# Kernel optimization log

Measured on AMD Instinct MI355X. Metric: run time of the kernel, lower is better.

The kernel has to match this reference:

```python
import jax, jax.numpy as jnp
import numpy as np

B, H, S, D = 2, 16, 2048, 64


def setup_inputs() -> dict:
    key = jax.random.key(0)
    kq, kk, kv = jax.random.split(key, 3)
    q = jax.random.normal(kq, (B, H, S, D), dtype=jnp.float32)
    k = jax.random.normal(kk, (B, H, S, D), dtype=jnp.float32)
    v = jax.random.normal(kv, (B, H, S, D), dtype=jnp.float32)
    # look-ahead (causal) mask: 1 where attention is NOT allowed (future positions)
    mask = 1.0 - jnp.tril(jnp.ones((S, S), dtype=jnp.float32))
    mask = mask[None, None, :, :]  # broadcastable to (B, H, S, S)
    return {"q": q, "k": k, "v": v, "mask": mask}


def reference(q, k, v, mask):
    # scores: (B, H, Sq, Sk)
    dk = jnp.asarray(q.shape[-1], dtype=q.dtype)
    logits = jnp.einsum("bhqd,bhkd->bhqk", q, k) / jnp.sqrt(dk)
    logits = logits + mask * (-1e9)
    attn = jax.nn.softmax(logits, axis=-1)
    # dropout rate 0.0 / inference mode -> identity
    out = jnp.einsum("bhqk,bhkd->bhqd", attn, v)
    return out, attn
```

## Files before the change

### kernel.cpp

```cpp
#include <hip/hip_runtime.h>


typedef __attribute__((ext_vector_type(4))) float f32x4;
typedef __attribute__((ext_vector_type(8))) short bf16x8;

#define S_LEN 2048
#define D_DIM 64
#define LDK   72
#define SCALE2 0.18033688f

__device__ __forceinline__ unsigned int f2bf1(float f) {
  unsigned int u = __float_as_uint(f);
  return (u + 0x7FFFu + ((u >> 16) & 1u)) >> 16;
}
__device__ __forceinline__ unsigned long long pack4bf(float a, float b, float c, float d) {
  unsigned int lo = f2bf1(a) | (f2bf1(b) << 16);
  unsigned int hi = f2bf1(c) | (f2bf1(d) << 16);
  return (unsigned long long)lo | ((unsigned long long)hi << 32);
}

__global__ __launch_bounds__(256, 2)
void attn_fused(const float* __restrict__ Qg, const float* __restrict__ Kg,
                const float* __restrict__ Vg, float* __restrict__ Og,
                float* __restrict__ Ag)
{
  __shared__ __attribute__((aligned(16))) unsigned short qs[64 * LDK];
  __shared__ __attribute__((aligned(16))) unsigned short ks[2][64 * LDK];
  __shared__ __attribute__((aligned(16))) unsigned short vs[2][64 * LDK];

  const int tid  = threadIdx.x;
  const int w    = tid >> 6;
  const int l15  = tid & 15;
  const int lg   = (tid >> 4) & 3;
  const int bh   = blockIdx.x & 31;
  const int pj   = blockIdx.x >> 5;

  const float* qb = Qg + (size_t)bh * S_LEN * D_DIM;
  const float* kb = Kg + (size_t)bh * S_LEN * D_DIM;
  const float* vb = Vg + (size_t)bh * S_LEN * D_DIM;
  float* ob = Og + (size_t)bh * S_LEN * D_DIM;
  float* ab = Ag + (size_t)bh * S_LEN * S_LEN;

  unsigned short* pw = qs + w * 16 * LDK;

  for (int sel = 0; sel < 2; ++sel) {
    const int jq   = sel ? (31 - pj) : pj;
    const int q0   = jq << 6;
    const int T    = jq + 1;
    const int qrow = q0 + w * 16 + l15;
    const int qr0  = q0 + w * 16 + lg * 4;

    __syncthreads();
#pragma unroll
    for (int jj = 0; jj < 4; ++jj) {
      int f = tid + jj * 256;
      int row = f >> 4, dg = f & 15;
      float4 v = *(const float4*)(qb + (q0 + row) * D_DIM + dg * 4);
      *(unsigned long long*)(qs + row * LDK + dg * 4) = pack4bf(v.x, v.y, v.z, v.w);
    }
#pragma unroll
    for (int jj = 0; jj < 4; ++jj) {
      int f = tid + jj * 256;
      int row = f >> 4, dg = f & 15;
      float4 v = *(const float4*)(kb + row * D_DIM + dg * 4);
      *(unsigned long long*)(ks[0] + row * LDK + dg * 4) = pack4bf(v.x, v.y, v.z, v.w);
    }
    __syncthreads();
    const bf16x8 qf0 = *(const bf16x8*)(qs + (w * 16 + l15) * LDK + lg * 8);
    const bf16x8 qf1 = *(const bf16x8*)(qs + (w * 16 + l15) * LDK + 32 + lg * 8);

    float lsum = 0.f;
    int cur = 0;

#define P1_KBK(MASKED)                                                                  \
    _Pragma("unroll")                                                                   \
    for (int kbk = 0; kbk < 4; ++kbk) {                                                 \
      const bf16x8 kf0 = *(const bf16x8*)(kcur + (kbk * 16 + l15) * LDK + lg * 8);      \
      const bf16x8 kf1 = *(const bf16x8*)(kcur + (kbk * 16 + l15) * LDK + 32 + lg * 8); \
      f32x4 s = {0.f, 0.f, 0.f, 0.f};                                                   \
      s = __builtin_amdgcn_mfma_f32_16x16x32_bf16(kf0, qf0, s, 0, 0, 0);                \
      s = __builtin_amdgcn_mfma_f32_16x16x32_bf16(kf1, qf1, s, 0, 0, 0);                \
      _Pragma("unroll")                                                                 \
      for (int r = 0; r < 4; ++r) {                                                     \
        float e = exp2f(s[r] * SCALE2);                                                 \
        if (MASKED) lsum += (kt + kbk * 16 + lg * 4 + r <= qrow) ? e : 0.f;             \
        else        lsum += e;                                                          \
      }                                                                                 \
    }

    for (int t = 0; t < T; ++t) {
      const int kt = t << 6;
      const bool pf = (t + 1 < T);
      float4 kl[4];
      if (pf) {
#pragma unroll
        for (int jj = 0; jj < 4; ++jj) {
          int f = tid + jj * 256;
          int row = f >> 4, dg = f & 15;
          kl[jj] = *(const float4*)(kb + (kt + 64 + row) * D_DIM + dg * 4);
        }
      }
      const unsigned short* kcur = ks[cur];
      if (t == T - 1) { P1_KBK(1) } else { P1_KBK(0) }
      if (pf) {
#pragma unroll
        for (int jj = 0; jj < 4; ++jj) {
          int f = tid + jj * 256;
          int row = f >> 4, dg = f & 15;
          *(unsigned long long*)(ks[cur ^ 1] + row * LDK + dg * 4) =
              pack4bf(kl[jj].x, kl[jj].y, kl[jj].z, kl[jj].w);
        }
      }
      __syncthreads();
      cur ^= 1;
    }
    lsum += __shfl_xor(lsum, 16, 64);
    lsum += __shfl_xor(lsum, 32, 64);
    const float ri = 1.f / lsum;

    f32x4 o[4];
#pragma unroll
    for (int d = 0; d < 4; ++d) o[d] = (f32x4){0.f, 0.f, 0.f, 0.f};

#pragma unroll
    for (int jj = 0; jj < 4; ++jj) {
      int f = tid + jj * 256;
      int row = f >> 4, dg = f & 15;
      float4 v = *(const float4*)(kb + row * D_DIM + dg * 4);
      *(unsigned long long*)(ks[0] + row * LDK + dg * 4) = pack4bf(v.x, v.y, v.z, v.w);
    }
    {
      const int kb4 = tid >> 4, db4 = tid & 15;
      const float* vsrc = vb + (kb4 * 4) * D_DIM + db4 * 4;
      float4 r0 = *(const float4*)(vsrc);
      float4 r1 = *(const float4*)(vsrc + D_DIM);
      float4 r2 = *(const float4*)(vsrc + 2 * D_DIM);
      float4 r3 = *(const float4*)(vsrc + 3 * D_DIM);
      *(unsigned long long*)(vs[0] + (db4 * 4 + 0) * LDK + kb4 * 4) = pack4bf(r0.x, r1.x, r2.x, r3.x);
      *(unsigned long long*)(vs[0] + (db4 * 4 + 1) * LDK + kb4 * 4) = pack4bf(r0.y, r1.y, r2.y, r3.y);
      *(unsigned long long*)(vs[0] + (db4 * 4 + 2) * LDK + kb4 * 4) = pack4bf(r0.z, r1.z, r2.z, r3.z);
      *(unsigned long long*)(vs[0] + (db4 * 4 + 3) * LDK + kb4 * 4) = pack4bf(r0.w, r1.w, r2.w, r3.w);
    }
    __syncthreads();

#define P2_KBK(MASKED)                                                                  \
    _Pragma("unroll")                                                                   \
    for (int kbk = 0; kbk < 4; ++kbk) {                                                 \
      const bf16x8 kf0 = *(const bf16x8*)(kcur + (kbk * 16 + l15) * LDK + lg * 8);      \
      const bf16x8 kf1 = *(const bf16x8*)(kcur + (kbk * 16 + l15) * LDK + 32 + lg * 8); \
      f32x4 s = {0.f, 0.f, 0.f, 0.f};                                                   \
      s = __builtin_amdgcn_mfma_f32_16x16x32_bf16(kf0, qf0, s, 0, 0, 0);                \
      s = __builtin_amdgcn_mfma_f32_16x16x32_bf16(kf1, qf1, s, 0, 0, 0);                \
      f32x4 pv;                                                                         \
      _Pragma("unroll")                                                                 \
      for (int r = 0; r < 4; ++r) {                                                     \
        float p = exp2f(s[r] * SCALE2) * ri;                                            \
        if (MASKED) p = (kt + kbk * 16 + lg * 4 + r <= qrow) ? p : 0.f;                 \
        pv[r] = p;                                                                      \
      }                                                                                 \
      __builtin_nontemporal_store(pv,                                                   \
        (f32x4*)(ab + (size_t)qrow * S_LEN + kt + kbk * 16 + lg * 4));                  \
      *(unsigned long long*)(pw + l15 * LDK + kbk * 16 + lg * 4) =                      \
          pack4bf(pv[0], pv[1], pv[2], pv[3]);                                          \
    }

    cur = 0;
    for (int t = 0; t < T; ++t) {
      const int kt = t << 6;
      const bool pf = (t + 1 < T);
      float4 kl[4], v0, v1, v2, v3;
      if (pf) {
#pragma unroll
        for (int jj = 0; jj < 4; ++jj) {
          int f = tid + jj * 256;
          int row = f >> 4, dg = f & 15;
          kl[jj] = *(const float4*)(kb + (kt + 64 + row) * D_DIM + dg * 4);
        }
        const int kb4 = tid >> 4, db4 = tid & 15;
        const float* vsrc = vb + (kt + 64 + kb4 * 4) * D_DIM + db4 * 4;
        v0 = *(const float4*)(vsrc);
        v1 = *(const float4*)(vsrc + D_DIM);
        v2 = *(const float4*)(vsrc + 2 * D_DIM);
        v3 = *(const float4*)(vsrc + 3 * D_DIM);
      }
      const unsigned short* kcur = ks[cur];
      if (t == T - 1) { P2_KBK(1) } else { P2_KBK(0) }
      asm volatile("s_waitcnt lgkmcnt(0)" ::: "memory");

      const bf16x8 pa0 = *(const bf16x8*)(pw + l15 * LDK + lg * 8);
      const bf16x8 pa1 = *(const bf16x8*)(pw + l15 * LDK + 32 + lg * 8);
      const unsigned short* vcur = vs[cur];
#pragma unroll
      for (int d = 0; d < 4; ++d) {
        const bf16x8 vf0 = *(const bf16x8*)(vcur + (d * 16 + l15) * LDK + lg * 8);
        const bf16x8 vf1 = *(const bf16x8*)(vcur + (d * 16 + l15) * LDK + 32 + lg * 8);
        o[d] = __builtin_amdgcn_mfma_f32_16x16x32_bf16(pa0, vf0, o[d], 0, 0, 0);
        o[d] = __builtin_amdgcn_mfma_f32_16x16x32_bf16(pa1, vf1, o[d], 0, 0, 0);
      }
      if (pf) {
#pragma unroll
        for (int jj = 0; jj < 4; ++jj) {
          int f = tid + jj * 256;
          int row = f >> 4, dg = f & 15;
          *(unsigned long long*)(ks[cur ^ 1] + row * LDK + dg * 4) =
              pack4bf(kl[jj].x, kl[jj].y, kl[jj].z, kl[jj].w);
        }
        const int kb4 = tid >> 4, db4 = tid & 15;
        *(unsigned long long*)(vs[cur ^ 1] + (db4 * 4 + 0) * LDK + kb4 * 4) = pack4bf(v0.x, v1.x, v2.x, v3.x);
        *(unsigned long long*)(vs[cur ^ 1] + (db4 * 4 + 1) * LDK + kb4 * 4) = pack4bf(v0.y, v1.y, v2.y, v3.y);
        *(unsigned long long*)(vs[cur ^ 1] + (db4 * 4 + 2) * LDK + kb4 * 4) = pack4bf(v0.z, v1.z, v2.z, v3.z);
        *(unsigned long long*)(vs[cur ^ 1] + (db4 * 4 + 3) * LDK + kb4 * 4) = pack4bf(v0.w, v1.w, v2.w, v3.w);
      }
      __syncthreads();
      cur ^= 1;
    }

    {
      const f32x4 z = (f32x4){0.f, 0.f, 0.f, 0.f};
#pragma unroll
      for (int jj = 0; jj < 4; ++jj) {
        const int zrow = q0 + w * 16 + jj * 4 + lg;
        float* rp = ab + (size_t)zrow * S_LEN;
        for (int c = q0 + 64 + l15 * 4; c < S_LEN; c += 64)
          __builtin_nontemporal_store(z, (f32x4*)(rp + c));
      }
    }

#pragma unroll
    for (int r = 0; r < 4; ++r) {
      float* rp = ob + (size_t)(qr0 + r) * D_DIM + l15;
      __builtin_nontemporal_store(o[0][r], rp);
      __builtin_nontemporal_store(o[1][r], rp + 16);
      __builtin_nontemporal_store(o[2][r], rp + 32);
      __builtin_nontemporal_store(o[3][r], rp + 48);
    }
  }
}

extern "C" void kernel_launch(void* const* d_in, const int* in_sizes, int n_in,
                              void* d_out, int out_size, void* d_ws, size_t ws_size,
                              hipStream_t stream) {
  (void)in_sizes; (void)n_in; (void)d_ws; (void)ws_size; (void)out_size;
  const float* q = (const float*)d_in[0];
  const float* k = (const float*)d_in[1];
  const float* v = (const float*)d_in[2];
  float* out  = (float*)d_out;
  float* attn = out + (size_t)2 * 16 * 2048 * 64;
  attn_fused<<<dim3(512), dim3(256), 0, stream>>>(q, k, v, out, attn);
}
```

Measured before the change: 170.3 us.

## Process both paired query tiles in one K/V sweep to share staged tiles

Each block now processes its two paired query tiles (pj and 31-pj) together in a single pass over the K and V tiles, instead of running the whole two-pass pipeline twice. Staged K/V tiles are loaded and converted once and serve both query tiles, which cuts global loads, bf16 conversions and barriers. The QK MFMA operand order is swapped so each lane's scores run along key columns, and the attention matrix is written as row-coalesced 16-byte stores read back from the bf16 P buffer in shared memory. It also remaps blockIdx to the pair index so heavy and light blocks interleave. The costs are roughly doubled register pressure (two accumulator sets and row sums) under launch bounds of 2 blocks per CU, and attention values are now stored rounded to bf16 rather than in fp32.

```diff
diff --git a/kernel.cpp b/kernel.cpp
--- a/kernel.cpp
+++ b/kernel.cpp
@@ -33,7 +33,17 @@
   const int l15  = tid & 15;
   const int lg   = (tid >> 4) & 3;
   const int bh   = blockIdx.x & 31;
-  const int pj   = blockIdx.x >> 5;
+  const int m    = blockIdx.x >> 5;
+  const int pj   = (m < 8) ? m : (23 - m);
+
+  const int jqA  = pj;
+  const int jqB  = 31 - pj;
+  const int q0A  = jqA << 6;
+  const int q0B  = jqB << 6;
+  const int TA   = jqA + 1;
+  const int TB   = jqB + 1;
+  const int qr0A = q0A + w * 16 + lg * 4;
+  const int qr0B = q0B + w * 16 + lg * 4;
 
   const float* qb = Qg + (size_t)bh * S_LEN * D_DIM;
   const float* kb = Kg + (size_t)bh * S_LEN * D_DIM;
@@ -43,197 +53,239 @@
 
   unsigned short* pw = qs + w * 16 * LDK;
 
-  for (int sel = 0; sel < 2; ++sel) {
-    const int jq   = sel ? (31 - pj) : pj;
-    const int q0   = jq << 6;
-    const int T    = jq + 1;
-    const int qrow = q0 + w * 16 + l15;
-    const int qr0  = q0 + w * 16 + lg * 4;
-
-    __syncthreads();
-#pragma unroll
-    for (int jj = 0; jj < 4; ++jj) {
-      int f = tid + jj * 256;
-      int row = f >> 4, dg = f & 15;
-      float4 v = *(const float4*)(qb + (q0 + row) * D_DIM + dg * 4);
-      *(unsigned long long*)(qs + row * LDK + dg * 4) = pack4bf(v.x, v.y, v.z, v.w);
-    }
-#pragma unroll
-    for (int jj = 0; jj < 4; ++jj) {
-      int f = tid + jj * 256;
-      int row = f >> 4, dg = f & 15;
-      float4 v = *(const float4*)(kb + row * D_DIM + dg * 4);
-      *(unsigned long long*)(ks[0] + row * LDK + dg * 4) = pack4bf(v.x, v.y, v.z, v.w);
-    }
-    __syncthreads();
-    const bf16x8 qf0 = *(const bf16x8*)(qs + (w * 16 + l15) * LDK + lg * 8);
-    const bf16x8 qf1 = *(const bf16x8*)(qs + (w * 16 + l15) * LDK + 32 + lg * 8);
-
-    float lsum = 0.f;
-    int cur = 0;
-
-#define P1_KBK(MASKED)                                                                  \
+#pragma unroll
+  for (int jj = 0; jj < 4; ++jj) {
+    int f = tid + jj * 256;
+    int row = f >> 4, dg = f & 15;
+    float4 v = *(const float4*)(qb + (q0A + row) * D_DIM + dg * 4);
+    *(unsigned long long*)(qs + row * LDK + dg * 4) = pack4bf(v.x, v.y, v.z, v.w);
+  }
+#pragma unroll
+  for (int jj = 0; jj < 4; ++jj) {
+    int f = tid + jj * 256;
+    int row = f >> 4, dg = f & 15;
+    float4 v = *(const float4*)(kb + row * D_DIM + dg * 4);
+    *(unsigned long long*)(ks[0] + row * LDK + dg * 4) = pack4bf(v.x, v.y, v.z, v.w);
+  }
+  __syncthreads();
+  const bf16x8 qfA0 = *(const bf16x8*)(qs + (w * 16 + l15) * LDK + lg * 8);
+  const bf16x8 qfA1 = *(const bf16x8*)(qs + (w * 16 + l15) * LDK + 32 + lg * 8);
+  __syncthreads();
+#pragma unroll
+  for (int jj = 0; jj < 4; ++jj) {
+    int f = tid + jj * 256;
+    int row = f >> 4, dg = f & 15;
+    float4 v = *(const float4*)(qb + (q0B + row) * D_DIM + dg * 4);
+    *(unsigned long long*)(qs + row * LDK + dg * 4) = pack4bf(v.x, v.y, v.z, v.w);
+  }
+  __syncthreads();
+  const bf16x8 qfB0 = *(const bf16x8*)(qs + (w * 16 + l15) * LDK + lg * 8);
+  const bf16x8 qfB1 = *(const bf16x8*)(qs + (w * 16 + l15) * LDK + 32 + lg * 8);
+
+#define P1_STEP(QF0, QF1, LSUM, QR0, MASKED)                                            \
+  {                                                                                     \
     _Pragma("unroll")                                                                   \
     for (int kbk = 0; kbk < 4; ++kbk) {                                                 \
       const bf16x8 kf0 = *(const bf16x8*)(kcur + (kbk * 16 + l15) * LDK + lg * 8);      \
       const bf16x8 kf1 = *(const bf16x8*)(kcur + (kbk * 16 + l15) * LDK + 32 + lg * 8); \
       f32x4 s = {0.f, 0.f, 0.f, 0.f};                                                   \
-      s = __builtin_amdgcn_mfma_f32_16x16x32_bf16(kf0, qf0, s, 0, 0, 0);                \
-      s = __builtin_amdgcn_mfma_f32_16x16x32_bf16(kf1, qf1, s, 0, 0, 0);                \
+      s = __builtin_amdgcn_mfma_f32_16x16x32_bf16(QF0, kf0, s, 0, 0, 0);                \
+      s = __builtin_amdgcn_mfma_f32_16x16x32_bf16(QF1, kf1, s, 0, 0, 0);                \
+      const int kc = kt + kbk * 16 + l15;                                               \
       _Pragma("unroll")                                                                 \
       for (int r = 0; r < 4; ++r) {                                                     \
         float e = exp2f(s[r] * SCALE2);                                                 \
-        if (MASKED) lsum += (kt + kbk * 16 + lg * 4 + r <= qrow) ? e : 0.f;             \
-        else        lsum += e;                                                          \
+        if (MASKED) LSUM[r] += (kc <= (QR0) + r) ? e : 0.f;                             \
+        else        LSUM[r] += e;                                                       \
       }                                                                                 \
-    }
-
-    for (int t = 0; t < T; ++t) {
-      const int kt = t << 6;
-      const bool pf = (t + 1 < T);
-      float4 kl[4];
-      if (pf) {
-#pragma unroll
-        for (int jj = 0; jj < 4; ++jj) {
-          int f = tid + jj * 256;
-          int row = f >> 4, dg = f & 15;
-          kl[jj] = *(const float4*)(kb + (kt + 64 + row) * D_DIM + dg * 4);
-        }
+    }                                                                                   \
+  }
+
+  float lsumA[4] = {0.f, 0.f, 0.f, 0.f};
+  float lsumB[4] = {0.f, 0.f, 0.f, 0.f};
+  int cur = 0;
+  for (int t = 0; t < TB; ++t) {
+    const int kt = t << 6;
+    const bool pf = (t + 1 < TB);
+    float4 kl[4];
+    if (pf) {
+#pragma unroll
+      for (int jj = 0; jj < 4; ++jj) {
+        int f = tid + jj * 256;
+        int row = f >> 4, dg = f & 15;
+        kl[jj] = *(const float4*)(kb + (kt + 64 + row) * D_DIM + dg * 4);
       }
-      const unsigned short* kcur = ks[cur];
-      if (t == T - 1) { P1_KBK(1) } else { P1_KBK(0) }
-      if (pf) {
-#pragma unroll
-        for (int jj = 0; jj < 4; ++jj) {
-          int f = tid + jj * 256;
-          int row = f >> 4, dg = f & 15;
-          *(unsigned long long*)(ks[cur ^ 1] + row * LDK + dg * 4) =
-              pack4bf(kl[jj].x, kl[jj].y, kl[jj].z, kl[jj].w);
-        }
+    }
+    const unsigned short* kcur = ks[cur];
+    if (t < TA) {
+      if (t == TA - 1) P1_STEP(qfA0, qfA1, lsumA, qr0A, 1)
+      else             P1_STEP(qfA0, qfA1, lsumA, qr0A, 0)
+    }
+    if (t == TB - 1) P1_STEP(qfB0, qfB1, lsumB, qr0B, 1)
+    else             P1_STEP(qfB0, qfB1, lsumB, qr0B, 0)
+    if (pf) {
+#pragma unroll
+      for (int jj = 0; jj < 4; ++jj) {
+        int f = tid + jj * 256;
+        int row = f >> 4, dg = f & 15;
+        *(unsigned long long*)(ks[cur ^ 1] + row * LDK + dg * 4) =
+            pack4bf(kl[jj].x, kl[jj].y, kl[jj].z, kl[jj].w);
       }
-      __syncthreads();
-      cur ^= 1;
-    }
-    lsum += __shfl_xor(lsum, 16, 64);
-    lsum += __shfl_xor(lsum, 32, 64);
-    const float ri = 1.f / lsum;
-
-    f32x4 o[4];
-#pragma unroll
-    for (int d = 0; d < 4; ++d) o[d] = (f32x4){0.f, 0.f, 0.f, 0.f};
-
-#pragma unroll
-    for (int jj = 0; jj < 4; ++jj) {
-      int f = tid + jj * 256;
-      int row = f >> 4, dg = f & 15;
-      float4 v = *(const float4*)(kb + row * D_DIM + dg * 4);
-      *(unsigned long long*)(ks[0] + row * LDK + dg * 4) = pack4bf(v.x, v.y, v.z, v.w);
-    }
-    {
-      const int kb4 = tid >> 4, db4 = tid & 15;
-      const float* vsrc = vb + (kb4 * 4) * D_DIM + db4 * 4;
-      float4 r0 = *(const float4*)(vsrc);
-      float4 r1 = *(const float4*)(vsrc + D_DIM);
-      float4 r2 = *(const float4*)(vsrc + 2 * D_DIM);
-      float4 r3 = *(const float4*)(vsrc + 3 * D_DIM);
-      *(unsigned long long*)(vs[0] + (db4 * 4 + 0) * LDK + kb4 * 4) = pack4bf(r0.x, r1.x, r2.x, r3.x);
-      *(unsigned long long*)(vs[0] + (db4 * 4 + 1) * LDK + kb4 * 4) = pack4bf(r0.y, r1.y, r2.y, r3.y);
-      *(unsigned long long*)(vs[0] + (db4 * 4 + 2) * LDK + kb4 * 4) = pack4bf(r0.z, r1.z, r2.z, r3.z);
-      *(unsigned long long*)(vs[0] + (db4 * 4 + 3) * LDK + kb4 * 4) = pack4bf(r0.w, r1.w, r2.w, r3.w);
     }
     __syncthreads();
-
-#define P2_KBK(MASKED)                                                                  \
+    cur ^= 1;
+  }
+#pragma unroll
+  for (int mm = 1; mm < 16; mm <<= 1) {
+#pragma unroll
+    for (int r = 0; r < 4; ++r) {
+      lsumA[r] += __shfl_xor(lsumA[r], mm, 64);
+      lsumB[r] += __shfl_xor(lsumB[r], mm, 64);
+    }
+  }
+  float riA[4], riB[4];
+#pragma unroll
+  for (int r = 0; r < 4; ++r) { riA[r] = 1.f / lsumA[r]; riB[r] = 1.f / lsumB[r]; }
+
+#define P2_STEP(QF0, QF1, RI, Q0, QR0, O, MASKED)                                       \
+  {                                                                                     \
     _Pragma("unroll")                                                                   \
     for (int kbk = 0; kbk < 4; ++kbk) {                                                 \
       const bf16x8 kf0 = *(const bf16x8*)(kcur + (kbk * 16 + l15) * LDK + lg * 8);      \
       const bf16x8 kf1 = *(const bf16x8*)(kcur + (kbk * 16 + l15) * LDK + 32 + lg * 8); \
       f32x4 s = {0.f, 0.f, 0.f, 0.f};                                                   \
-      s = __builtin_amdgcn_mfma_f32_16x16x32_bf16(kf0, qf0, s, 0, 0, 0);                \
-      s = __builtin_amdgcn_mfma_f32_16x16x32_bf16(kf1, qf1, s, 0, 0, 0);                \
-      f32x4 pv;                                                                         \
+      s = __builtin_amdgcn_mfma_f32_16x16x32_bf16(QF0, kf0, s, 0, 0, 0);                \
+      s = __builtin_amdgcn_mfma_f32_16x16x32_bf16(QF1, kf1, s, 0, 0, 0);                \
+      const int kc = kt + kbk * 16 + l15;                                               \
       _Pragma("unroll")                                                                 \
       for (int r = 0; r < 4; ++r) {                                                     \
-        float p = exp2f(s[r] * SCALE2) * ri;                                            \
-        if (MASKED) p = (kt + kbk * 16 + lg * 4 + r <= qrow) ? p : 0.f;                 \
-        pv[r] = p;                                                                      \
+        float p = exp2f(s[r] * SCALE2) * RI[r];                                         \
+        if (MASKED) p = (kc <= (QR0) + r) ? p : 0.f;                                    \
+        pw[(lg * 4 + r) * LDK + kbk * 16 + l15] = (unsigned short)f2bf1(p);             \
       }                                                                                 \
-      __builtin_nontemporal_store(pv,                                                   \
-        (f32x4*)(ab + (size_t)qrow * S_LEN + kt + kbk * 16 + lg * 4));                  \
-      *(unsigned long long*)(pw + l15 * LDK + kbk * 16 + lg * 4) =                      \
-          pack4bf(pv[0], pv[1], pv[2], pv[3]);                                          \
-    }
-
-    cur = 0;
-    for (int t = 0; t < T; ++t) {
-      const int kt = t << 6;
-      const bool pf = (t + 1 < T);
-      float4 kl[4], v0, v1, v2, v3;
-      if (pf) {
-#pragma unroll
-        for (int jj = 0; jj < 4; ++jj) {
-          int f = tid + jj * 256;
-          int row = f >> 4, dg = f & 15;
-          kl[jj] = *(const float4*)(kb + (kt + 64 + row) * D_DIM + dg * 4);
-        }
-        const int kb4 = tid >> 4, db4 = tid & 15;
-        const float* vsrc = vb + (kt + 64 + kb4 * 4) * D_DIM + db4 * 4;
-        v0 = *(const float4*)(vsrc);
-        v1 = *(const float4*)(vsrc + D_DIM);
-        v2 = *(const float4*)(vsrc + 2 * D_DIM);
-        v3 = *(const float4*)(vsrc + 3 * D_DIM);
+    }                                                                                   \
+    asm volatile("s_waitcnt lgkmcnt(0)" ::: "memory");                                  \
+    _Pragma("unroll")                                                                   \
+    for (int jj = 0; jj < 4; ++jj) {                                                    \
+      const int row = jj * 4 + lg;                                                      \
+      uint2 pk2 = *(const uint2*)(pw + row * LDK + l15 * 4);                            \
+      f32x4 fv;                                                                         \
+      fv.x = __uint_as_float((pk2.x & 0xFFFFu) << 16);                                  \
+      fv.y = __uint_as_float(pk2.x & 0xFFFF0000u);                                      \
+      fv.z = __uint_as_float((pk2.y & 0xFFFFu) << 16);                                  \
+      fv.w = __uint_as_float(pk2.y & 0xFFFF0000u);                                      \
+      __builtin_nontemporal_store(fv,                                                   \
+        (f32x4*)(ab + (size_t)((Q0) + w * 16 + row) * S_LEN + kt + l15 * 4));           \
+    }                                                                                   \
+    const bf16x8 pa0 = *(const bf16x8*)(pw + l15 * LDK + lg * 8);                       \
+    const bf16x8 pa1 = *(const bf16x8*)(pw + l15 * LDK + 32 + lg * 8);                  \
+    _Pragma("unroll")                                                                   \
+    for (int d = 0; d < 4; ++d) {                                                       \
+      const bf16x8 vf0 = *(const bf16x8*)(vcur + (d * 16 + l15) * LDK + lg * 8);        \
+      const bf16x8 vf1 = *(const bf16x8*)(vcur + (d * 16 + l15) * LDK + 32 + lg * 8);   \
+      O[d] = __builtin_amdgcn_mfma_f32_16x16x32_bf16(pa0, vf0, O[d], 0, 0, 0);          \
+      O[d] = __builtin_amdgcn_mfma_f32_16x16x32_bf16(pa1, vf1, O[d], 0, 0, 0);          \
+    }                                                                                   \
+  }
+
+  f32x4 oA[4], oB[4];
+#pragma unroll
+  for (int d = 0; d < 4; ++d) { oA[d] = (f32x4){0.f,0.f,0.f,0.f}; oB[d] = (f32x4){0.f,0.f,0.f,0.f}; }
+
+  __syncthreads();
+#pragma unroll
+  for (int jj = 0; jj < 4; ++jj) {
+    int f = tid + jj * 256;
+    int row = f >> 4, dg = f & 15;
+    float4 v = *(const float4*)(kb + row * D_DIM + dg * 4);
+    *(unsigned long long*)(ks[0] + row * LDK + dg * 4) = pack4bf(v.x, v.y, v.z, v.w);
+  }
+  {
+    const int kb4 = tid >> 4, db4 = tid & 15;
+    const float* vsrc = vb + (kb4 * 4) * D_DIM + db4 * 4;
+    float4 r0 = *(const float4*)(vsrc);
+    float4 r1 = *(const float4*)(vsrc + D_DIM);
+    float4 r2 = *(const float4*)(vsrc + 2 * D_DIM);
+    float4 r3 = *(const float4*)(vsrc + 3 * D_DIM);
+    *(unsigned long long*)(vs[0] + (db4 * 4 + 0) * LDK + kb4 * 4) = pack4bf(r0.x, r1.x, r2.x, r3.x);
+    *(unsigned long long*)(vs[0] + (db4 * 4 + 1) * LDK + kb4 * 4) = pack4bf(r0.y, r1.y, r2.y, r3.y);
+    *(unsigned long long*)(vs[0] + (db4 * 4 + 2) * LDK + kb4 * 4) = pack4bf(r0.z, r1.z, r2.z, r3.z);
+    *(unsigned long long*)(vs[0] + (db4 * 4 + 3) * LDK + kb4 * 4) = pack4bf(r0.w, r1.w, r2.w, r3.w);
+  }
+  __syncthreads();
+
+  cur = 0;
+  for (int t = 0; t < TB; ++t) {
+    const int kt = t << 6;
+    const bool pf = (t + 1 < TB);
+    float4 kl[4], v0, v1, v2, v3;
+    if (pf) {
+#pragma unroll
+      for (int jj = 0; jj < 4; ++jj) {
+        int f = tid + jj * 256;
+        int row = f >> 4, dg = f & 15;
+        kl[jj] = *(const float4*)(kb + (kt + 64 + row) * D_DIM + dg * 4);
       }
-      const unsigned short* kcur = ks[cur];
-      if (t == T - 1) { P2_KBK(1) } else { P2_KBK(0) }
-      asm volatile("s_waitcnt lgkmcnt(0)" ::: "memory");
-
-      const bf16x8 pa0 = *(const bf16x8*)(pw + l15 * LDK + lg * 8);
-      const bf16x8 pa1 = *(const bf16x8*)(pw + l15 * LDK + 32 + lg * 8);
-      const unsigned short* vcur = vs[cur];
-#pragma unroll
-      for (int d = 0; d < 4; ++d) {
-        const bf16x8 vf0 = *(const bf16x8*)(vcur + (d * 16 + l15) * LDK + lg * 8);
-        const bf16x8 vf1 = *(const bf16x8*)(vcur + (d * 16 + l15) * LDK + 32 + lg * 8);
-        o[d] = __builtin_amdgcn_mfma_f32_16x16x32_bf16(pa0, vf0, o[d], 0, 0, 0);
-        o[d] = __builtin_amdgcn_mfma_f32_16x16x32_bf16(pa1, vf1, o[d], 0, 0, 0);
+      const int kb4 = tid >> 4, db4 = tid & 15;
+      const float* vsrc = vb + (kt + 64 + kb4 * 4) * D_DIM + db4 * 4;
+      v0 = *(const float4*)(vsrc);
+      v1 = *(const float4*)(vsrc + D_DIM);
+      v2 = *(const float4*)(vsrc + 2 * D_DIM);
+      v3 = *(const float4*)(vsrc + 3 * D_DIM);
+    }
+    const unsigned short* kcur = ks[cur];
+    const unsigned short* vcur = vs[cur];
+    if (t < TA) {
+      if (t == TA - 1) P2_STEP(qfA0, qfA1, riA, q0A, qr0A, oA, 1)
+      else             P2_STEP(qfA0, qfA1, riA, q0A, qr0A, oA, 0)
+    }
+    if (t == TB - 1) P2_STEP(qfB0, qfB1, riB, q0B, qr0B, oB, 1)
+    else             P2_STEP(qfB0, qfB1, riB, q0B, qr0B, oB, 0)
+    if (pf) {
+#pragma unroll
+      for (int jj = 0; jj < 4; ++jj) {
+        int f = tid + jj * 256;
+        int row = f >> 4, dg = f & 15;
+        *(unsigned long long*)(ks[cur ^ 1] + row * LDK + dg * 4) =
+            pack4bf(kl[jj].x, kl[jj].y, kl[jj].z, kl[jj].w);
       }
-      if (pf) {
-#pragma unroll
-        for (int jj = 0; jj < 4; ++jj) {
-          int f = tid + jj * 256;
-          int row = f >> 4, dg = f & 15;
-          *(unsigned long long*)(ks[cur ^ 1] + row * LDK + dg * 4) =
-              pack4bf(kl[jj].x, kl[jj].y, kl[jj].z, kl[jj].w);
-        }
-        const int kb4 = tid >> 4, db4 = tid & 15;
-        *(unsigned long long*)(vs[cur ^ 1] + (db4 * 4 + 0) * LDK + kb4 * 4) = pack4bf(v0.x, v1.x, v2.x, v3.x);
-        *(unsigned long long*)(vs[cur ^ 1] + (db4 * 4 + 1) * LDK + kb4 * 4) = pack4bf(v0.y, v1.y, v2.y, v3.y);
-        *(unsigned long long*)(vs[cur ^ 1] + (db4 * 4 + 2) * LDK + kb4 * 4) = pack4bf(v0.z, v1.z, v2.z, v3.z);
-        *(unsigned long long*)(vs[cur ^ 1] + (db4 * 4 + 3) * LDK + kb4 * 4) = pack4bf(v0.w, v1.w, v2.w, v3.w);
-      }
-      __syncthreads();
-      cur ^= 1;
-    }
-
-    {
-      const f32x4 z = (f32x4){0.f, 0.f, 0.f, 0.f};
-#pragma unroll
-      for (int jj = 0; jj < 4; ++jj) {
-        const int zrow = q0 + w * 16 + jj * 4 + lg;
-        float* rp = ab + (size_t)zrow * S_LEN;
-        for (int c = q0 + 64 + l15 * 4; c < S_LEN; c += 64)
-          __builtin_nontemporal_store(z, (f32x4*)(rp + c));
-      }
-    }
-
-#pragma unroll
-    for (int r = 0; r < 4; ++r) {
-      float* rp = ob + (size_t)(qr0 + r) * D_DIM + l15;
-      __builtin_nontemporal_store(o[0][r], rp);
-      __builtin_nontemporal_store(o[1][r], rp + 16);
-      __builtin_nontemporal_store(o[2][r], rp + 32);
-      __builtin_nontemporal_store(o[3][r], rp + 48);
-    }
+      const int kb4 = tid >> 4, db4 = tid & 15;
+      *(unsigned long long*)(vs[cur ^ 1] + (db4 * 4 + 0) * LDK + kb4 * 4) = pack4bf(v0.x, v1.x, v2.x, v3.x);
+      *(unsigned long long*)(vs[cur ^ 1] + (db4 * 4 + 1) * LDK + kb4 * 4) = pack4bf(v0.y, v1.y, v2.y, v3.y);
+      *(unsigned long long*)(vs[cur ^ 1] + (db4 * 4 + 2) * LDK + kb4 * 4) = pack4bf(v0.z, v1.z, v2.z, v3.z);
+      *(unsigned long long*)(vs[cur ^ 1] + (db4 * 4 + 3) * LDK + kb4 * 4) = pack4bf(v0.w, v1.w, v2.w, v3.w);
+    }
+    __syncthreads();
+    cur ^= 1;
+  }
+
+  {
+    const f32x4 z = (f32x4){0.f, 0.f, 0.f, 0.f};
+#pragma unroll
+    for (int jj = 0; jj < 4; ++jj) {
+      const int rowA = q0A + w * 16 + jj * 4 + lg;
+      float* rpA = ab + (size_t)rowA * S_LEN;
+      for (int c = q0A + 64 + l15 * 4; c < S_LEN; c += 64)
+        __builtin_nontemporal_store(z, (f32x4*)(rpA + c));
+      const int rowB = q0B + w * 16 + jj * 4 + lg;
+      float* rpB = ab + (size_t)rowB * S_LEN;
+      for (int c = q0B + 64 + l15 * 4; c < S_LEN; c += 64)
+        __builtin_nontemporal_store(z, (f32x4*)(rpB + c));
+    }
+  }
+
+#pragma unroll
+  for (int r = 0; r < 4; ++r) {
+    float* rpA = ob + (size_t)(qr0A + r) * D_DIM + l15;
+    __builtin_nontemporal_store(oA[0][r], rpA);
+    __builtin_nontemporal_store(oA[1][r], rpA + 16);
+    __builtin_nontemporal_store(oA[2][r], rpA + 32);
+    __builtin_nontemporal_store(oA[3][r], rpA + 48);
+    float* rpB = ob + (size_t)(qr0B + r) * D_DIM + l15;
+    __builtin_nontemporal_store(oB[0][r], rpB);
+    __builtin_nontemporal_store(oB[1][r], rpB + 16);
+    __builtin_nontemporal_store(oB[2][r], rpB + 32);
+    __builtin_nontemporal_store(oB[3][r], rpB + 48);
   }
 }
 
```

Result: no change. 169.1 us (-0.7%).
